# Kernel optimization log

Measured on AMD Instinct MI355X. Metric: run time of the kernel, lower is better.

Reference implementation:

```python
import jax, jax.numpy as jnp
import numpy as np

EPS_GN = 1e-8
EPS_ATTN = 1e-8


def setup_inputs() -> dict:
    key = jax.random.key(0)
    ks = jax.random.split(key, 13)
    B, C, N = 4, 512, 2048
    s = 0.02
    return {
        "x": jax.random.normal(ks[0], (B, C, N), jnp.float32),
        "dw_w": jax.random.normal(ks[1], (C, 3), jnp.float32) * s,
        "pw_w": jax.random.normal(ks[2], (C, C), jnp.float32) * s,
        "u_w": jax.random.normal(ks[3], (2 * C, C), jnp.float32) * s,
        "u_b": jax.random.normal(ks[4], (2 * C,), jnp.float32) * s,
        "v_w": jax.random.normal(ks[5], (2 * C, C), jnp.float32) * s,
        "v_b": jax.random.normal(ks[6], (2 * C,), jnp.float32) * s,
        "h_w": jax.random.normal(ks[7], (C, C), jnp.float32) * s,
        "h_b": jax.random.normal(ks[8], (C,), jnp.float32) * s,
        "q_w": jax.random.normal(ks[9], (C, C), jnp.float32) * s,
        "k_w": jax.random.normal(ks[10], (C, C), jnp.float32) * s,
        "o_w": jax.random.normal(ks[11], (C, 2 * C), jnp.float32) * s,
        "o_b": jax.random.normal(ks[12], (C,), jnp.float32) * s,
    }


def reference(x, dw_w, pw_w, u_w, u_b, v_w, v_b, h_w, h_b, q_w, k_w, o_w, o_b):
    # x: [B, C, N]
    C = x.shape[1]
    # GroupNorm(1, C): normalize over (C, N) per sample; affine is identity-init
    # in torch but we follow the module math with default weight=1, bias=0
    mean = jnp.mean(x, axis=(1, 2), keepdims=True)
    var = jnp.var(x, axis=(1, 2), keepdims=True)
    z = (x - mean) * jax.lax.rsqrt(var + EPS_GN)

    # local depthwise conv k=3, pad=1 (cross-correlation), no bias
    zp = jnp.pad(z, ((0, 0), (0, 0), (1, 1)))
    dw = (dw_w[:, 0, None] * zp[:, :, :-2]
          + dw_w[:, 1, None] * zp[:, :, 1:-1]
          + dw_w[:, 2, None] * zp[:, :, 2:])
    # pointwise conv (no bias)
    z = z + jnp.einsum('oc,bcn->bon', pw_w, dw)

    u = jax.nn.sigmoid(jnp.einsum('oc,bcn->bon', u_w, z) + u_b[:, None])  # [B,2C,N]
    v = jnp.einsum('oc,bcn->bon', v_w, z) + v_b[:, None]                  # [B,2C,N]
    h = jnp.einsum('oc,bcn->bno', h_w, z) + h_b                           # [B,N,C]

    q = h @ q_w.T  # [B,N,C]
    k = h @ k_w.T  # [B,N,C]
    scale = 1.0 / jnp.sqrt(jnp.float32(C))

    logits = jnp.einsum('bnc,bmc->bnm', q, k) * scale
    a = jax.nn.relu(logits)
    a = a * a
    a = a / (jnp.sum(a, axis=-1, keepdims=True) + EPS_ATTN)

    av = jnp.einsum('bnm,bom->bon', a, v)  # [B,2C,N]
    y = jnp.einsum('oc,bcn->bon', o_w, u * av) + o_b[:, None]
    return x + y
```

## Files before the change

### kernel.cpp

```cpp
#include <hip/hip_runtime.h>
#include <hip/hip_bf16.h>
#include <cstdint>

typedef __bf16 bhalf;
typedef __bf16 bhalf8 __attribute__((ext_vector_type(8)));
typedef float f32x4 __attribute__((ext_vector_type(4)));

enum { EPI_Z2=0, EPI_UV=1, EPI_BIAS=2, EPI_QK=3, EPI_ATTN=4, EPI_PV=5, EPI_Y=6, EPI_ST=7 };

__device__ __forceinline__ void gl_lds16(const void* g, void* l) {
  __builtin_amdgcn_global_load_lds(
      (const __attribute__((address_space(1))) unsigned int*)g,
      (__attribute__((address_space(3))) unsigned int*)l,
      16, 0, 0);
}
__device__ __forceinline__ void barrier_raw() { asm volatile("s_barrier" ::: "memory"); }
#define VMW(n)  asm volatile("s_waitcnt vmcnt(" #n ")" ::: "memory")
#define LGKM0() asm volatile("s_waitcnt lgkmcnt(0)" ::: "memory")

__device__ __forceinline__ unsigned char to_fp8(float v){
  return (unsigned char)(__builtin_amdgcn_cvt_pk_fp8_f32(v, v, 0, false) & 0xff);
}


template<int EPI>
__global__ void __launch_bounds__(512, 2)
gA(const bhalf* __restrict__ A, const bhalf* __restrict__ Bw,
   void* __restrict__ Out, void* __restrict__ Out2,
   const float* __restrict__ bias, const float* __restrict__ bias2,
   int N, int K, long sA, long sB, long sO, long sAuxf, float scale)
{
  constexpr int KSL = 256*64;
  constexpr int REG = 2*KSL;
  constexpr int DBUF = 2*REG;
  __shared__ __align__(16) char lds[2*DBUF];

  const int gx = gridDim.x, gy = gridDim.y;
  const int nwg = gx*gy;
  const int flat = blockIdx.y*gx + blockIdx.x;
  const int q8 = nwg>>3, r8 = nwg&7, xcd = flat&7, o8 = flat>>3;
  const int wsw = (xcd<r8 ? xcd*(q8+1) : r8*(q8+1)+(xcd-r8)*q8) + o8;
  const int bx = wsw % gx, by = wsw / gx;
  const int m0 = by*256, n0 = bx*256;
  const int bz = blockIdx.z;

  const bhalf* Ab = A + (long)bz*sA;
  const bhalf* Bb = Bw + (long)bz*sB;

  const int tid = threadIdx.x, wid = tid>>6, lane = tid&63;
  const int lm = lane&15, kq = lane>>4;
  const int wm = wid>>2, wn = wid&3;
  const int srow = lane>>2;
  const int csw = ((lane&3) ^ ((lane>>3)&3)) * 8;
  const int kqs = kq ^ ((lm>>1)&3);

  f32x4 acc[8][4];
  #pragma unroll
  for (int i=0;i<8;i++)
    #pragma unroll
    for (int j=0;j<4;j++) acc[i][j] = f32x4{0.f,0.f,0.f,0.f};

  auto stageA = [&](int kt){
    char* base = lds + (kt&1)*DBUF;
    const int k0 = kt*64;
    #pragma unroll
    for (int h=0; h<2; h++)
      #pragma unroll
      for (int ksl=0; ksl<2; ksl++){
        bhalf* d = (bhalf*)(base + ksl*KSL + (h*128 + wid*16)*64);
        gl_lds16(Ab + (long)(m0 + h*128 + wid*16 + srow)*K + k0 + ksl*32 + csw, d);
      }
  };
  auto stageB = [&](int kt){
    char* base = lds + (kt&1)*DBUF + REG;
    const int k0 = kt*64;
    #pragma unroll
    for (int h=0; h<2; h++)
      #pragma unroll
      for (int ksl=0; ksl<2; ksl++){
        bhalf* d = (bhalf*)(base + ksl*KSL + (h*128 + wid*16)*64);
        gl_lds16(Bb + (long)(n0 + h*128 + wid*16 + srow)*K + k0 + ksl*32 + csw, d);
      }
  };

  bhalf8 af[4][2], bf[4][2];
  auto readA = [&](int kt, int ih){
    char* base = lds + (kt&1)*DBUF;
    #pragma unroll
    for (int i2=0;i2<4;i2++)
      #pragma unroll
      for (int ksl=0;ksl<2;ksl++)
        af[i2][ksl] = *(const bhalf8*)(base + ksl*KSL + (wm*128 + ih*64 + i2*16 + lm)*64 + kqs*16);
  };
  auto readB = [&](int kt, int jh){
    char* base = lds + (kt&1)*DBUF + REG;
    #pragma unroll
    for (int j2=0;j2<2;j2++)
      #pragma unroll
      for (int ksl=0;ksl<2;ksl++)
        bf[jh*2+j2][ksl] = *(const bhalf8*)(base + ksl*KSL + (wn*64 + jh*32 + j2*16 + lm)*64 + kqs*16);
  };
  auto mfma16 = [&](int ih, int jh){
    __builtin_amdgcn_s_setprio(1);
    #pragma unroll
    for (int i2=0;i2<4;i2++)
      #pragma unroll
      for (int j2=0;j2<2;j2++)
        #pragma unroll
        for (int ksl=0;ksl<2;ksl++)
          acc[ih*4+i2][jh*2+j2] = __builtin_amdgcn_mfma_f32_16x16x32_bf16(
              af[i2][ksl], bf[jh*2+j2][ksl], acc[ih*4+i2][jh*2+j2], 0,0,0);
    __builtin_amdgcn_s_setprio(0);
  };

  const int NT = K>>6;
  stageA(0); stageB(0); stageA(1);
  for (int kt=0; kt<NT; ++kt){
    if (kt==NT-1) { VMW(0); } else { VMW(4); }
    barrier_raw();
    readA(kt,0); readB(kt,0);
    if (kt+1<NT) stageB(kt+1);
    mfma16(0,0);
    barrier_raw();
    readB(kt,1);
    mfma16(0,1);
    barrier_raw();
    readA(kt,1);
    mfma16(1,0);
    barrier_raw();
    if (kt+2<NT) stageA(kt+2);
    mfma16(1,1);
  }
  barrier_raw();

  if constexpr (EPI==EPI_ATTN){
    float rs[8][4];
    #pragma unroll
    for (int i=0;i<8;i++)
      #pragma unroll
      for (int r=0;r<4;r++) rs[i][r]=0.f;
    #pragma unroll
    for (int i=0;i<8;i++){
      #pragma unroll
      for (int j=0;j<4;j++){
        const int lcol = wn*64 + j*16 + lm;
        #pragma unroll
        for (int r=0;r<4;r++){
          const int lrow = wm*128 + i*16 + kq*4 + r;
          float v = acc[i][j][r];
          v *= scale; v = fmaxf(v,0.f); v = v*v;
          rs[i][r] += v;
          const int lb = lrow*256 + ((((lcol>>4) ^ (lrow&15)))<<4) + (lcol&15);
          *(unsigned char*)(lds + lb) = to_fp8(v);
        }
      }
    }
    float* rd = (float*)Out2;
    #pragma unroll
    for (int i=0;i<8;i++){
      const int rbase = m0 + wm*128 + i*16 + kq*4;
      #pragma unroll
      for (int r=0;r<4;r++){
        float s = rs[i][r];
        s += __shfl_xor(s,1); s += __shfl_xor(s,2);
        s += __shfl_xor(s,4); s += __shfl_xor(s,8);
        if (lm==0) atomicAdd(rd + (long)bz*sAuxf + rbase + r, s);
      }
    }
    LGKM0();
    barrier_raw();
    char* obase = (char*)Out + (long)bz*sO + (long)m0*N + n0;
    #pragma unroll
    for (int it=0; it<8; ++it){
      const int g = (it*512 + tid)*16;
      const int row = g >> 8, off = g & 255;
      const int lb = row*256 + ((((off>>4) ^ (row&15)))<<4);
      uint4 val = *(const uint4*)(lds + lb);
      *(uint4*)(obase + (long)row*N + off) = val;
    }
  }
  if constexpr (EPI==EPI_UV){
    const bool uh = n0 < 1024;
    const float* bv = uh ? bias : bias2;
    const int bc0 = uh ? n0 : n0-1024;
    #pragma unroll
    for (int i=0;i<8;i++){
      #pragma unroll
      for (int j=0;j<4;j++){
        const int lcol = wn*64 + j*16 + lm;
        #pragma unroll
        for (int r=0;r<4;r++){
          const int lrow = wm*128 + i*16 + kq*4 + r;
          float v = acc[i][j][r] + bv[bc0 + lcol];
          if (uh){
            v = 1.f/(1.f + __expf(-v));
            const int cb = lcol*2;
            const int lb = lrow*512 + (((cb>>5) ^ ((lrow>>2)&3))<<5) + (cb&31);
            *(bhalf*)(lds + lb) = (bhalf)v;
          } else {
            const int lb = lcol*256 + ((((lrow>>4) ^ (lcol&15)))<<4) + (lrow&15);
            *(unsigned char*)(lds + lb) = to_fp8(v);
          }
        }
      }
    }
    LGKM0();
    barrier_raw();
    if (uh){
      char* obase = (char*)Out + 2*((long)m0*1024 + n0);
      #pragma unroll
      for (int it=0; it<16; ++it){
        const int g = (it*512 + tid)*16;
        const int row = g >> 9, off = g & 511;
        const int lb = row*512 + (((off>>5) ^ ((row>>2)&3))<<5) + (off&31);
        uint4 val = *(const uint4*)(lds + lb);
        *(uint4*)(obase + (long)row*2048 + off) = val;
      }
    } else {
      char* vb = (char*)Out2 + ((long)(m0>>11)*1024*2048 + (long)(n0-1024)*2048 + (m0 & 2047));
      #pragma unroll
      for (int it=0; it<8; ++it){
        const int g = (it*512 + tid)*16;
        const int row = g >> 8, off = g & 255;
        const int lb = row*256 + ((((off>>4) ^ (row&15)))<<4);
        uint4 val = *(const uint4*)(lds + lb);
        *(uint4*)(vb + (long)row*2048 + off) = val;
      }
    }
  }
  (void)scale; (void)bias; (void)bias2; (void)N;
}

__global__ void __launch_bounds__(256, 2)
g4k8(const unsigned char* __restrict__ A, const unsigned char* __restrict__ Bw,
     bhalf* __restrict__ Out,
     const bhalf* __restrict__ ub, const float* __restrict__ rden,
     int K, long sB, int rowshift)
{
  constexpr int DBUF = 256*64;
  __shared__ __align__(16) char lds[4*DBUF];

  const int gx = gridDim.x, gy = gridDim.y;
  const int nwg = gx*gy;
  const int flat = blockIdx.y*gx + blockIdx.x;
  const int q8 = nwg>>3, r8 = nwg&7, xcd = flat&7, o8 = flat>>3;
  const int w = (xcd<r8 ? xcd*(q8+1) : r8*(q8+1)+(xcd-r8)*q8) + o8;
  const int bx = w % gx, by = w / gx;
  const int m0 = by*128, n0 = bx*128;

  const unsigned char* Bb = Bw + (long)(m0>>rowshift)*sB;

  const int tid = threadIdx.x;
  const int wid = tid>>6, lane = tid&63;
  const int lm = lane&15, kq = lane>>4;
  const int wm = wid>>1, wn = wid&1;
  const int srow = lane>>2;
  const int csw8 = ((lane&3) ^ ((lane>>3)&3))*16;
  int coff[2];
  #pragma unroll
  for (int ksl=0; ksl<2; ksl++)
    coff[ksl] = ((((ksl*2 + (kq>>1)) ^ ((lm>>1)&3)))<<4) + ((kq&1)<<3);

  f32x4 acc[4][4];
  #pragma unroll
  for (int i=0;i<4;i++)
    #pragma unroll
    for (int j=0;j<4;j++) acc[i][j] = f32x4{0.f,0.f,0.f,0.f};

  auto stage = [&](int kt){
    char* base = lds + (kt&3)*DBUF;
    const int k0 = kt*64;
    #pragma unroll
    for (int c=0;c<4;c++){
      const int r0 = c*64 + wid*16;
      char* d = base + r0*64;
      const unsigned char* g = (r0 < 128)
        ? A  + (long)(m0 + r0 + srow)*K + k0 + csw8
        : Bb + (long)(n0 + r0 - 128 + srow)*K + k0 + csw8;
      gl_lds16(g, d);
    }
  };

  long af[4][2], bf[4][2];
  auto readA = [&](int kt){
    char* base = lds + (kt&3)*DBUF;
    #pragma unroll
    for (int i2=0;i2<4;i2++)
      #pragma unroll
      for (int ksl=0;ksl<2;ksl++)
        af[i2][ksl] = *(const long*)(base + (wm*64 + i2*16 + lm)*64 + coff[ksl]);
  };
  auto readB = [&](int kt, int jh){
    char* base = lds + (kt&3)*DBUF;
    #pragma unroll
    for (int j2=0;j2<2;j2++)
      #pragma unroll
      for (int ksl=0;ksl<2;ksl++)
        bf[jh*2+j2][ksl] = *(const long*)(base + (128 + wn*64 + jh*32 + j2*16 + lm)*64 + coff[ksl]);
  };
  auto mfma16 = [&](int jh){
    __builtin_amdgcn_s_setprio(1);
    #pragma unroll
    for (int i2=0;i2<4;i2++)
      #pragma unroll
      for (int j2=0;j2<2;j2++)
        #pragma unroll
        for (int ksl=0;ksl<2;ksl++)
          acc[i2][jh*2+j2] = __builtin_amdgcn_mfma_f32_16x16x32_fp8_fp8(
              af[i2][ksl], bf[jh*2+j2][ksl], acc[i2][jh*2+j2], 0,0,0);
    __builtin_amdgcn_s_setprio(0);
  };

  const int NT = K>>6;
  stage(0); stage(1); stage(2);
  for (int kt=0; kt<NT; ++kt){
    if (kt==NT-1)      { VMW(0); }
    else if (kt==NT-2) { VMW(4); }
    else               { VMW(8); }
    barrier_raw();
    readA(kt); readB(kt,0);
    if (kt+3<NT) stage(kt+3);
    mfma16(0);
    readB(kt,1);
    mfma16(1);
  }
  barrier_raw();

  char* obase = (char*)Out + 2*((long)m0*1024 + n0);
  #pragma unroll
  for (int i=0;i<4;i++){
    #pragma unroll
    for (int j=0;j<4;j++){
      const int lcol = wn*64 + j*16 + lm;
      #pragma unroll
      for (int r=0;r<4;r++){
        const int lrow = wm*64 + i*16 + kq*4 + r;
        const int rowg = m0 + lrow;
        float v = acc[i][j][r];
        float den = rden[rowg];
        v *= __builtin_amdgcn_rcpf(den + 1e-8f);
        v *= (float)ub[(long)rowg*1024 + n0 + lcol];
        const int cb = lcol*2;
        const int lb = lrow*256 + (((cb>>5) ^ ((lrow>>2)&3))<<5) + (cb&31);
        *(bhalf*)(lds + lb) = (bhalf)v;
      }
    }
  }
  LGKM0();
  barrier_raw();
  #pragma unroll
  for (int it=0; it<8; ++it){
    const int g = (it*256 + tid)*16;
    const int row = g >> 8, off = g & 255;
    const int lb = row*256 + (((off>>5) ^ ((row>>2)&3))<<5) + (off&31);
    uint4 val = *(const uint4*)(lds + lb);
    *(uint4*)(obase + (long)row*2048 + off) = val;
  }
}

template<int EPI>
__global__ void __launch_bounds__(256, 2)
g4k(const bhalf* __restrict__ A, const bhalf* __restrict__ Bw,
    void* __restrict__ Out, void* __restrict__ Out2,
    const float* __restrict__ bias,
    const bhalf* __restrict__ auxb,
    const float* __restrict__ xadd,
    int M, int N, int K)
{
  constexpr int KSL = 256*64;
  constexpr int DBUF = 2*KSL;
  __shared__ __align__(16) char lds[2*DBUF];

  const int gx = gridDim.x, gy = gridDim.y;
  const int nwg = gx*gy;
  const int flat = blockIdx.y*gx + blockIdx.x;
  const int q8 = nwg>>3, r8 = nwg&7, xcd = flat&7, o8 = flat>>3;
  const int w = (xcd<r8 ? xcd*(q8+1) : r8*(q8+1)+(xcd-r8)*q8) + o8;
  const int bx = w % gx, by = w / gx;
  const int m0 = by*128, n0 = bx*128;

  const int tid = threadIdx.x;
  const int wid = tid>>6, lane = tid&63;
  const int lm = lane&15, kq = lane>>4;
  const int wm = wid>>1, wn = wid&1;
  const int srow = lane>>2;
  const int csw = ((lane&3) ^ ((lane>>3)&3))*8;
  const int kqs = kq ^ ((lm>>1)&3);

  f32x4 acc[4][4];
  #pragma unroll
  for (int i=0;i<4;i++)
    #pragma unroll
    for (int j=0;j<4;j++) acc[i][j] = f32x4{0.f,0.f,0.f,0.f};

  auto stage = [&](int kt){
    char* base = lds + (kt&1)*DBUF;
    const int k0 = kt*64;
    #pragma unroll
    for (int c=0;c<4;c++){
      const int r0 = c*64 + wid*16;
      #pragma unroll
      for (int ksl=0; ksl<2; ksl++){
        bhalf* d = (bhalf*)(base + ksl*KSL + r0*64);
        const bhalf* g = (r0 < 128)
          ? A  + (long)(m0 + r0 + srow)*K + k0 + ksl*32 + csw
          : Bw + (long)(n0 + r0 - 128 + srow)*K + k0 + ksl*32 + csw;
        gl_lds16(g, d);
      }
    }
  };

  bhalf8 af[4][2], bf[4][2];
  auto readA = [&](int kt){
    char* base = lds + (kt&1)*DBUF;
    #pragma unroll
    for (int i2=0;i2<4;i2++)
      #pragma unroll
      for (int ksl=0;ksl<2;ksl++)
        af[i2][ksl] = *(const bhalf8*)(base + ksl*KSL + (wm*64 + i2*16 + lm)*64 + kqs*16);
  };
  auto readB = [&](int kt, int jh){
    char* base = lds + (kt&1)*DBUF;
    #pragma unroll
    for (int j2=0;j2<2;j2++)
      #pragma unroll
      for (int ksl=0;ksl<2;ksl++)
        bf[jh*2+j2][ksl] = *(const bhalf8*)(base + ksl*KSL + (128 + wn*64 + jh*32 + j2*16 + lm)*64 + kqs*16);
  };
  auto mfma16 = [&](int jh){
    __builtin_amdgcn_s_setprio(1);
    #pragma unroll
    for (int i2=0;i2<4;i2++)
      #pragma unroll
      for (int j2=0;j2<2;j2++)
        #pragma unroll
        for (int ksl=0;ksl<2;ksl++)
          acc[i2][jh*2+j2] = __builtin_amdgcn_mfma_f32_16x16x32_bf16(
              af[i2][ksl], bf[jh*2+j2][ksl], acc[i2][jh*2+j2], 0,0,0);
    __builtin_amdgcn_s_setprio(0);
  };

  const int NT = K>>6;
  stage(0); stage(1);
  for (int kt=0; kt<NT; ++kt){
    if (kt==NT-1) { VMW(0); } else { VMW(8); }
    barrier_raw();
    readA(kt); readB(kt,0);
    mfma16(0);
    barrier_raw();
    readB(kt,1);
    if (kt+2<NT) stage(kt+2);
    mfma16(1);
  }
  barrier_raw();

  if constexpr (EPI==EPI_Y){
    #pragma unroll
    for (int i=0;i<4;i++){
      #pragma unroll
      for (int j=0;j<4;j++){
        const int lcol = wn*64 + j*16 + lm;
        #pragma unroll
        for (int r=0;r<4;r++){
          const int lrow = wm*64 + i*16 + kq*4 + r;
          float v = acc[i][j][r] + bias[n0 + lcol];
          const int lb = lcol*512 + 4*(lrow ^ ((lcol&15)<<2));
          *(float*)(lds + lb) = v;
        }
      }
    }
    LGKM0();
    barrier_raw();
    const int b = m0 >> 11, nb = m0 & 2047;
    float* ob = (float*)Out + ((long)b*512 + n0)*2048 + nb;
    const float* xb = xadd + ((long)b*512 + n0)*2048 + nb;
    #pragma unroll
    for (int it=0; it<16; ++it){
      const int g = (it*256 + tid)*16;
      const int row = g >> 9, off = g & 511;
      const int t0 = off >> 2;
      const int s = (row&15)<<2;
      f32x4 vv = *(const f32x4*)(lds + row*512 + 4*(t0^s));
      f32x4 xx = *(const f32x4*)(xb + (long)row*2048 + t0);
      *(f32x4*)(ob + (long)row*2048 + t0) = vv + xx;
    }
  } else {
    char* obase; int ldb;
    if constexpr (EPI==EPI_QK){
      bool qh = n0 < 512;
      obase = (char*)(qh?Out:Out2) + 2*((long)m0*512 + (n0 - (qh?0:512)));
      ldb = 1024;
    } else {
      obase = (char*)Out + 2*((long)m0*N + n0);
      ldb = N*2;
    }
    #pragma unroll
    for (int i=0;i<4;i++){
      #pragma unroll
      for (int j=0;j<4;j++){
        const int lcol = wn*64 + j*16 + lm;
        #pragma unroll
        for (int r=0;r<4;r++){
          const int lrow = wm*64 + i*16 + kq*4 + r;
          float v = acc[i][j][r];
          if constexpr (EPI==EPI_Z2)
            v += (float)auxb[(long)(m0+lrow)*N + n0 + lcol];
          if constexpr (EPI==EPI_BIAS)
            v += bias[n0 + lcol];
          if constexpr (EPI==EPI_QK)
            v += bias[n0 + lcol];
          const int cb = lcol*2;
          const int lb = lrow*256 + (((cb>>5) ^ ((lrow>>2)&3))<<5) + (cb&31);
          *(bhalf*)(lds + lb) = (bhalf)v;
        }
      }
    }
    LGKM0();
    barrier_raw();
    #pragma unroll
    for (int it=0; it<8; ++it){
      const int g = (it*256 + tid)*16;
      const int row = g >> 8, off = g & 255;
      const int lb = row*256 + (((off>>5) ^ ((row>>2)&3))<<5) + (off&31);
      uint4 val = *(const uint4*)(lds + lb);
      *(uint4*)(obase + (long)row*ldb + off) = val;
    }
  }
  (void)M; (void)xadd; (void)bias; (void)auxb;
}

struct CvtArgs { const float* src[7]; bhalf* dst[7]; int n[7]; };
__global__ void cvt_multi(CvtArgs a) {
  int seg = blockIdx.y;
  int i = (blockIdx.x*256 + threadIdx.x)*4;
  if (i >= a.n[seg]) return;
  float4 f = *(const float4*)(a.src[seg] + i);
  bhalf* d = a.dst[seg] + i;
  d[0]=(bhalf)f.x; d[1]=(bhalf)f.y; d[2]=(bhalf)f.z; d[3]=(bhalf)f.w;
}

__global__ void transpose_bf16(const bhalf* __restrict__ in, bhalf* __restrict__ out,
                               int R, int C) {
  __shared__ bhalf t[32][33];
  int r0 = blockIdx.x*32, c0 = blockIdx.y*32;
  int tx = threadIdx.x, ty = threadIdx.y;
  #pragma unroll
  for (int r=0;r<4;r++)
    t[ty + r*8][tx] = in[(long)(r0 + ty + r*8)*C + c0 + tx];
  __syncthreads();
  #pragma unroll
  for (int r=0;r<4;r++)
    out[(long)(c0 + ty + r*8)*R + r0 + tx] = t[tx][ty + r*8];
}

__global__ void qk_bias(const bhalf* __restrict__ wqk, const float* __restrict__ hb,
                        float* __restrict__ bq){
  int row = blockIdx.x*4 + (threadIdx.x>>6);
  int lane = threadIdx.x & 63;
  const bhalf* p = wqk + (long)row*512;
  float s = 0.f;
  #pragma unroll
  for (int j=0;j<8;j++) s += (float)p[lane*8+j] * hb[lane*8+j];
  for (int off=32; off; off>>=1) s += __shfl_xor(s, off);
  if (lane==0) bq[row] = s;
}

__global__ void gn_part(const float* __restrict__ x, float* __restrict__ ps, float* __restrict__ pss) {
  int b = blockIdx.y;
  const float* xb = x + (long)b*(512*2048);
  float s=0.f, ss=0.f;
  #pragma unroll
  for (int it=0; it<8; it++){
    int idx = ((it*128 + blockIdx.x)*256 + threadIdx.x)*4;
    float4 f = *(const float4*)(xb + idx);
    s  += f.x+f.y+f.z+f.w;
    ss += f.x*f.x+f.y*f.y+f.z*f.z+f.w*f.w;
  }
  for (int off=32; off; off>>=1){ s += __shfl_xor(s,off); ss += __shfl_xor(ss,off); }
  __shared__ float ls[4], lss[4];
  int wid = threadIdx.x>>6, lane = threadIdx.x&63;
  if (lane==0){ ls[wid]=s; lss[wid]=ss; }
  __syncthreads();
  if (threadIdx.x==0){
    s = ls[0]+ls[1]+ls[2]+ls[3]; ss = lss[0]+lss[1]+lss[2]+lss[3];
    ps[b*128 + blockIdx.x] = s; pss[b*128 + blockIdx.x] = ss;
  }
}

__global__ void gn_final(const float* __restrict__ ps, const float* __restrict__ pss,
                         float* __restrict__ stats) {
  int b = blockIdx.x;
  float s = ps[b*128 + threadIdx.x], ss = pss[b*128 + threadIdx.x];
  for (int off=32; off; off>>=1){ s += __shfl_xor(s,off); ss += __shfl_xor(ss,off); }
  __shared__ float l0[2], l1[2];
  int wid = threadIdx.x>>6, lane = threadIdx.x&63;
  if (lane==0){ l0[wid]=s; l1[wid]=ss; }
  __syncthreads();
  if (threadIdx.x==0){
    s = l0[0]+l0[1]; ss = l1[0]+l1[1];
    float mean = s*(1.f/1048576.f);
    float var  = ss*(1.f/1048576.f) - mean*mean;
    stats[b*2] = mean; stats[b*2+1] = rsqrtf(var + 1e-8f);
  }
}

__global__ void norm_dw_T(const float* __restrict__ x, const float* __restrict__ stats,
                          const float* __restrict__ dw_w,
                          bhalf* __restrict__ zT, bhalf* __restrict__ dwT) {
  int b = blockIdx.z, n0 = blockIdx.x*32, c0 = blockIdx.y*32;
  float mean = stats[b*2], rstd = stats[b*2+1];
  __shared__ float zs[32][35];
  int tx = threadIdx.x, ty = threadIdx.y;
  #pragma unroll
  for (int r=0;r<4;r++){
    int c = c0 + ty + r*8;
    for (int cc=tx; cc<34; cc+=32){
      int n = n0 - 1 + cc;
      float v = 0.f;
      if (n>=0 && n<2048) v = (x[((long)b*512 + c)*2048 + n] - mean)*rstd;
      zs[ty + r*8][cc] = v;
    }
  }
  __syncthreads();
  float w0 = dw_w[(c0+tx)*3+0], w1 = dw_w[(c0+tx)*3+1], w2 = dw_w[(c0+tx)*3+2];
  #pragma unroll
  for (int r=0;r<4;r++){
    int ln = ty + r*8;
    float z = zs[tx][ln+1];
    float d = w0*zs[tx][ln] + w1*zs[tx][ln+1] + w2*zs[tx][ln+2];
    long o = ((long)b*2048 + n0 + ln)*512 + c0 + tx;
    zT[o] = (bhalf)z; dwT[o] = (bhalf)d;
  }
}

extern "C" void kernel_launch(void* const* d_in, const int* in_sizes, int n_in,
                              void* d_out, int out_size, void* d_ws, size_t ws_size,
                              hipStream_t stream) {
  (void)in_sizes; (void)n_in; (void)out_size; (void)ws_size;
  const float* x    = (const float*)d_in[0];
  const float* dw_w = (const float*)d_in[1];
  const float* pw_w = (const float*)d_in[2];
  const float* u_w  = (const float*)d_in[3];
  const float* u_b  = (const float*)d_in[4];
  const float* v_w  = (const float*)d_in[5];
  const float* v_b  = (const float*)d_in[6];
  const float* h_w  = (const float*)d_in[7];
  const float* h_b  = (const float*)d_in[8];
  const float* q_w  = (const float*)d_in[9];
  const float* k_w  = (const float*)d_in[10];
  const float* o_w  = (const float*)d_in[11];
  const float* o_b  = (const float*)d_in[12];
  float* out = (float*)d_out;

  char* ws = (char*)d_ws;
  size_t off = 0;
  auto alloc = [&](size_t bytes) -> void* {
    void* p = ws + off; off = (off + bytes + 255) & ~(size_t)255; return p;
  };

  float* ps    = (float*)alloc(4*128*4);
  float* pss   = (float*)alloc(4*128*4);
  float* stats = (float*)alloc(4*2*4);
  float* rden  = (float*)alloc(4*2048*4);
  float* bq    = (float*)alloc(1024*4);
  bhalf* wb_pw = (bhalf*)alloc(512*512*2);
  bhalf* wb_uv = (bhalf*)alloc((size_t)2048*512*2);
  bhalf* wb_h  = (bhalf*)alloc(512*512*2);
  bhalf* hwT   = (bhalf*)alloc(512*512*2);
  bhalf* wb_qk = (bhalf*)alloc((size_t)1024*512*2);
  bhalf* wqk2  = (bhalf*)alloc((size_t)1024*512*2);
  bhalf* wb_o  = (bhalf*)alloc((size_t)512*1024*2);
  const size_t ACT = (size_t)4*2048*512;
  bhalf* zT   = (bhalf*)alloc(ACT*2);
  bhalf* dwT  = (bhalf*)alloc(ACT*2);
  bhalf* z2T  = (bhalf*)alloc(ACT*2);
  bhalf* ub   = (bhalf*)alloc(ACT*2*2);
  unsigned char* v_fm = (unsigned char*)alloc((size_t)4*1024*2048);
  unsigned char* wsc  = (unsigned char*)alloc((size_t)4*2048*2048);
  bhalf* uav  = (bhalf*)alloc(ACT*2*2);
  bhalf* qb = zT;  bhalf* kb = dwT;

  hipMemsetAsync(rden, 0, 4*2048*4, stream);

  CvtArgs ca;
  ca.src[0]=pw_w; ca.dst[0]=wb_pw;           ca.n[0]=512*512;
  ca.src[1]=u_w;  ca.dst[1]=wb_uv;           ca.n[1]=1024*512;
  ca.src[2]=v_w;  ca.dst[2]=wb_uv+1024*512;  ca.n[2]=1024*512;
  ca.src[3]=h_w;  ca.dst[3]=wb_h;            ca.n[3]=512*512;
  ca.src[4]=q_w;  ca.dst[4]=wb_qk;           ca.n[4]=512*512;
  ca.src[5]=k_w;  ca.dst[5]=wb_qk+512*512;   ca.n[5]=512*512;
  ca.src[6]=o_w;  ca.dst[6]=wb_o;            ca.n[6]=512*1024;
  cvt_multi<<<dim3(512,7), 256, 0, stream>>>(ca);

  transpose_bf16<<<dim3(16,16), dim3(32,8), 0, stream>>>(wb_h, hwT, 512, 512);
  g4k<EPI_ST><<<dim3(4,8,1), 256, 0, stream>>>(wb_qk, hwT, wqk2, nullptr,
      nullptr, nullptr, nullptr, 1024, 512, 512);
  qk_bias<<<dim3(256), 256, 0, stream>>>(wb_qk, h_b, bq);

  gn_part<<<dim3(128,4), 256, 0, stream>>>(x, ps, pss);
  gn_final<<<dim3(4), 128, 0, stream>>>(ps, pss, stats);

  norm_dw_T<<<dim3(64,16,4), dim3(32,8), 0, stream>>>(x, stats, dw_w, zT, dwT);

  const float iscl = 0.044194173824159216f;
  g4k<EPI_Z2><<<dim3(4,64,1), 256, 0, stream>>>(dwT, wb_pw, z2T, nullptr,
      nullptr, zT, nullptr, 8192, 512, 512);
  gA<EPI_UV><<<dim3(8,32,1), 512, 0, stream>>>(z2T, wb_uv, ub, v_fm,
      u_b, v_b, 2048, 512, 0, 0, 0, 0, 0.f);
  g4k<EPI_QK><<<dim3(8,64,1), 256, 0, stream>>>(z2T, wqk2, qb, kb,
      bq, nullptr, nullptr, 8192, 1024, 512);
  gA<EPI_ATTN><<<dim3(8,8,4), 512, 0, stream>>>(qb, kb, wsc, rden,
      nullptr, nullptr, 2048, 512,
      (long)2048*512, (long)2048*512, (long)2048*2048, 2048, iscl);
  g4k8<<<dim3(8,64,1), 256, 0, stream>>>(wsc, v_fm, uav, ub, rden,
      2048, (long)1024*2048, 11);
  g4k<EPI_Y><<<dim3(4,64,1), 256, 0, stream>>>(uav, wb_o, out, nullptr,
      o_b, nullptr, x, 8192, 512, 1024);
}
```

Before: 178.0 us.

## Store Q/K in fp8 and compute attention scores with new fp8 MFMA kernel

The QK projection epilogue now writes Q and K as fp8 instead of bf16, and a new gsc8 kernel computes the relu-squared score tiles with fp8 16x16x32 MFMAs on 128x128 tiles, triple-buffered in LDS. This replaces the bf16 gA<EPI_ATTN> path, halving Q/K traffic and using faster fp8 matrix instructions. The tile shape also shrinks to 128x128 with 256 threads, which gives more workgroups. It costs extra accuracy loss from quantizing Q and K to fp8 and adds two new buffers.

```diff
diff --git a/kernel.cpp b/kernel.cpp
--- a/kernel.cpp
+++ b/kernel.cpp
@@ -133,52 +133,6 @@
   }
   barrier_raw();
 
-  if constexpr (EPI==EPI_ATTN){
-    float rs[8][4];
-    #pragma unroll
-    for (int i=0;i<8;i++)
-      #pragma unroll
-      for (int r=0;r<4;r++) rs[i][r]=0.f;
-    #pragma unroll
-    for (int i=0;i<8;i++){
-      #pragma unroll
-      for (int j=0;j<4;j++){
-        const int lcol = wn*64 + j*16 + lm;
-        #pragma unroll
-        for (int r=0;r<4;r++){
-          const int lrow = wm*128 + i*16 + kq*4 + r;
-          float v = acc[i][j][r];
-          v *= scale; v = fmaxf(v,0.f); v = v*v;
-          rs[i][r] += v;
-          const int lb = lrow*256 + ((((lcol>>4) ^ (lrow&15)))<<4) + (lcol&15);
-          *(unsigned char*)(lds + lb) = to_fp8(v);
-        }
-      }
-    }
-    float* rd = (float*)Out2;
-    #pragma unroll
-    for (int i=0;i<8;i++){
-      const int rbase = m0 + wm*128 + i*16 + kq*4;
-      #pragma unroll
-      for (int r=0;r<4;r++){
-        float s = rs[i][r];
-        s += __shfl_xor(s,1); s += __shfl_xor(s,2);
-        s += __shfl_xor(s,4); s += __shfl_xor(s,8);
-        if (lm==0) atomicAdd(rd + (long)bz*sAuxf + rbase + r, s);
-      }
-    }
-    LGKM0();
-    barrier_raw();
-    char* obase = (char*)Out + (long)bz*sO + (long)m0*N + n0;
-    #pragma unroll
-    for (int it=0; it<8; ++it){
-      const int g = (it*512 + tid)*16;
-      const int row = g >> 8, off = g & 255;
-      const int lb = row*256 + ((((off>>4) ^ (row&15)))<<4);
-      uint4 val = *(const uint4*)(lds + lb);
-      *(uint4*)(obase + (long)row*N + off) = val;
-    }
-  }
   if constexpr (EPI==EPI_UV){
     const bool uh = n0 < 1024;
     const float* bv = uh ? bias : bias2;
@@ -228,7 +182,147 @@
       }
     }
   }
-  (void)scale; (void)bias; (void)bias2; (void)N;
+  (void)scale; (void)bias; (void)bias2; (void)N; (void)sO; (void)sAuxf;
+}
+
+__global__ void __launch_bounds__(256, 2)
+gsc8(const unsigned char* __restrict__ Q, const unsigned char* __restrict__ Kp,
+     unsigned char* __restrict__ Wsc, float* __restrict__ rden, float scale)
+{
+  constexpr int DBUF = 256*64;
+  __shared__ __align__(16) char lds[3*DBUF];
+
+  const int gx = gridDim.x, gy = gridDim.y;
+  const int nwg = gx*gy;
+  const int flat = blockIdx.y*gx + blockIdx.x;
+  const int q8 = nwg>>3, r8 = nwg&7, xcd = flat&7, o8 = flat>>3;
+  const int w = (xcd<r8 ? xcd*(q8+1) : r8*(q8+1)+(xcd-r8)*q8) + o8;
+  const int bx = w % gx, by = w / gx;
+  const int m0 = by*128, n0 = bx*128;
+  const int bz = blockIdx.z;
+  const int K = 512;
+
+  const unsigned char* Ab = Q  + (long)bz*2048*512;
+  const unsigned char* Bb = Kp + (long)bz*2048*512;
+
+  const int tid = threadIdx.x;
+  const int wid = tid>>6, lane = tid&63;
+  const int lm = lane&15, kq = lane>>4;
+  const int wm = wid>>1, wn = wid&1;
+  const int srow = lane>>2;
+  const int csw8 = ((lane&3) ^ ((lane>>3)&3))*16;
+  int coff[2];
+  #pragma unroll
+  for (int ksl=0; ksl<2; ksl++)
+    coff[ksl] = ((((ksl*2 + (kq>>1)) ^ ((lm>>1)&3)))<<4) + ((kq&1)<<3);
+
+  f32x4 acc[4][4];
+  #pragma unroll
+  for (int i=0;i<4;i++)
+    #pragma unroll
+    for (int j=0;j<4;j++) acc[i][j] = f32x4{0.f,0.f,0.f,0.f};
+
+  auto stage = [&](int kt){
+    char* base = lds + (kt%3)*DBUF;
+    const int k0 = kt*64;
+    #pragma unroll
+    for (int c=0;c<4;c++){
+      const int r0 = c*64 + wid*16;
+      char* d = base + r0*64;
+      const unsigned char* g = (r0 < 128)
+        ? Ab + (long)(m0 + r0 + srow)*K + k0 + csw8
+        : Bb + (long)(n0 + r0 - 128 + srow)*K + k0 + csw8;
+      gl_lds16(g, d);
+    }
+  };
+
+  long af[4][2], bf[4][2];
+  auto readA = [&](int kt){
+    char* base = lds + (kt%3)*DBUF;
+    #pragma unroll
+    for (int i2=0;i2<4;i2++)
+      #pragma unroll
+      for (int ksl=0;ksl<2;ksl++)
+        af[i2][ksl] = *(const long*)(base + (wm*64 + i2*16 + lm)*64 + coff[ksl]);
+  };
+  auto readB = [&](int kt, int jh){
+    char* base = lds + (kt%3)*DBUF;
+    #pragma unroll
+    for (int j2=0;j2<2;j2++)
+      #pragma unroll
+      for (int ksl=0;ksl<2;ksl++)
+        bf[jh*2+j2][ksl] = *(const long*)(base + (128 + wn*64 + jh*32 + j2*16 + lm)*64 + coff[ksl]);
+  };
+  auto mfma16 = [&](int jh){
+    __builtin_amdgcn_s_setprio(1);
+    #pragma unroll
+    for (int i2=0;i2<4;i2++)
+      #pragma unroll
+      for (int j2=0;j2<2;j2++)
+        #pragma unroll
+        for (int ksl=0;ksl<2;ksl++)
+          acc[i2][jh*2+j2] = __builtin_amdgcn_mfma_f32_16x16x32_fp8_fp8(
+              af[i2][ksl], bf[jh*2+j2][ksl], acc[i2][jh*2+j2], 0,0,0);
+    __builtin_amdgcn_s_setprio(0);
+  };
+
+  const int NT = 8;
+  stage(0); stage(1);
+  for (int kt=0; kt<NT; ++kt){
+    if (kt==NT-1) { VMW(0); } else { VMW(4); }
+    barrier_raw();
+    readA(kt); readB(kt,0);
+    if (kt+2<NT) stage(kt+2);
+    mfma16(0);
+    readB(kt,1);
+    mfma16(1);
+  }
+  barrier_raw();
+
+  float rs[4][4];
+  #pragma unroll
+  for (int i=0;i<4;i++)
+    #pragma unroll
+    for (int r=0;r<4;r++) rs[i][r]=0.f;
+  #pragma unroll
+  for (int i=0;i<4;i++){
+    #pragma unroll
+    for (int j=0;j<4;j++){
+      const int lcol = wn*64 + j*16 + lm;
+      #pragma unroll
+      for (int r=0;r<4;r++){
+        const int lrow = wm*64 + i*16 + kq*4 + r;
+        float v = acc[i][j][r];
+        v *= scale; v = fmaxf(v,0.f); v = v*v;
+        rs[i][r] += v;
+        const int lb = lrow*128 + ((((lcol>>4) ^ (lrow&7)))<<4) + (lcol&15);
+        *(unsigned char*)(lds + lb) = to_fp8(v);
+      }
+    }
+  }
+  float* rd = rden + (long)bz*2048;
+  #pragma unroll
+  for (int i=0;i<4;i++){
+    const int rbase = m0 + wm*64 + i*16 + kq*4;
+    #pragma unroll
+    for (int r=0;r<4;r++){
+      float s = rs[i][r];
+      s += __shfl_xor(s,1); s += __shfl_xor(s,2);
+      s += __shfl_xor(s,4); s += __shfl_xor(s,8);
+      if (lm==0) atomicAdd(rd + rbase + r, s);
+    }
+  }
+  LGKM0();
+  barrier_raw();
+  unsigned char* obase = Wsc + (long)bz*2048*2048 + (long)m0*2048 + n0;
+  #pragma unroll
+  for (int it=0; it<4; ++it){
+    const int g = (it*256 + tid)*16;
+    const int row = g >> 7, off = g & 127;
+    const int lb = row*128 + ((((off>>4) ^ (row&7)))<<4);
+    uint4 val = *(const uint4*)(lds + lb);
+    *(uint4*)(obase + (long)row*2048 + off) = val;
+  }
 }
 
 __global__ void __launch_bounds__(256, 2)
@@ -484,16 +578,36 @@
       f32x4 xx = *(const f32x4*)(xb + (long)row*2048 + t0);
       *(f32x4*)(ob + (long)row*2048 + t0) = vv + xx;
     }
+  } else if constexpr (EPI==EPI_QK){
+    bool qh = n0 < 512;
+    unsigned char* obase = (unsigned char*)(qh?Out:Out2) + (long)m0*512 + (n0 - (qh?0:512));
+    #pragma unroll
+    for (int i=0;i<4;i++){
+      #pragma unroll
+      for (int j=0;j<4;j++){
+        const int lcol = wn*64 + j*16 + lm;
+        #pragma unroll
+        for (int r=0;r<4;r++){
+          const int lrow = wm*64 + i*16 + kq*4 + r;
+          float v = acc[i][j][r] + bias[n0 + lcol];
+          const int lb = lrow*128 + ((((lcol>>4) ^ (lrow&7)))<<4) + (lcol&15);
+          *(unsigned char*)(lds + lb) = to_fp8(v);
+        }
+      }
+    }
+    LGKM0();
+    barrier_raw();
+    #pragma unroll
+    for (int it=0; it<4; ++it){
+      const int g = (it*256 + tid)*16;
+      const int row = g >> 7, off = g & 127;
+      const int lb = row*128 + ((((off>>4) ^ (row&7)))<<4);
+      uint4 val = *(const uint4*)(lds + lb);
+      *(uint4*)(obase + (long)row*512 + off) = val;
+    }
   } else {
-    char* obase; int ldb;
-    if constexpr (EPI==EPI_QK){
-      bool qh = n0 < 512;
-      obase = (char*)(qh?Out:Out2) + 2*((long)m0*512 + (n0 - (qh?0:512)));
-      ldb = 1024;
-    } else {
-      obase = (char*)Out + 2*((long)m0*N + n0);
-      ldb = N*2;
-    }
+    char* obase = (char*)Out + 2*((long)m0*N + n0);
+    const int ldb = N*2;
     #pragma unroll
     for (int i=0;i<4;i++){
       #pragma unroll
@@ -506,8 +620,6 @@
           if constexpr (EPI==EPI_Z2)
             v += (float)auxb[(long)(m0+lrow)*N + n0 + lcol];
           if constexpr (EPI==EPI_BIAS)
-            v += bias[n0 + lcol];
-          if constexpr (EPI==EPI_QK)
             v += bias[n0 + lcol];
           const int cb = lcol*2;
           const int lb = lrow*256 + (((cb>>5) ^ ((lrow>>2)&3))<<5) + (cb&31);
@@ -677,8 +789,9 @@
   bhalf* ub   = (bhalf*)alloc(ACT*2*2);
   unsigned char* v_fm = (unsigned char*)alloc((size_t)4*1024*2048);
   unsigned char* wsc  = (unsigned char*)alloc((size_t)4*2048*2048);
+  unsigned char* qb8  = (unsigned char*)alloc(ACT);
+  unsigned char* kb8  = (unsigned char*)alloc(ACT);
   bhalf* uav  = (bhalf*)alloc(ACT*2*2);
-  bhalf* qb = zT;  bhalf* kb = dwT;
 
   hipMemsetAsync(rden, 0, 4*2048*4, stream);
 
@@ -707,11 +820,9 @@
       nullptr, zT, nullptr, 8192, 512, 512);
   gA<EPI_UV><<<dim3(8,32,1), 512, 0, stream>>>(z2T, wb_uv, ub, v_fm,
       u_b, v_b, 2048, 512, 0, 0, 0, 0, 0.f);
-  g4k<EPI_QK><<<dim3(8,64,1), 256, 0, stream>>>(z2T, wqk2, qb, kb,
+  g4k<EPI_QK><<<dim3(8,64,1), 256, 0, stream>>>(z2T, wqk2, qb8, kb8,
       bq, nullptr, nullptr, 8192, 1024, 512);
-  gA<EPI_ATTN><<<dim3(8,8,4), 512, 0, stream>>>(qb, kb, wsc, rden,
-      nullptr, nullptr, 2048, 512,
-      (long)2048*512, (long)2048*512, (long)2048*2048, 2048, iscl);
+  gsc8<<<dim3(16,16,4), 256, 0, stream>>>(qb8, kb8, wsc, rden, iscl);
   g4k8<<<dim3(8,64,1), 256, 0, stream>>>(wsc, v_fm, uav, ub, rden,
       2048, (long)1024*2048, 11);
   g4k<EPI_Y><<<dim3(4,64,1), 256, 0, stream>>>(uav, wb_o, out, nullptr,
```

Measured after the change: 176.3 us. About the same (-1.0%).
